# Kernel tuning notes

Hardware: AMD Instinct MI355X
Metric: run time of the kernel (lower is better)

## Reference

```python
import jax, jax.numpy as jnp
import numpy as np

N, D_IN, D_KQ, D_V = 4096, 1024, 1024, 1024


def setup_inputs() -> dict:
    key = jax.random.key(0)
    kx, kq, kk, kv = jax.random.split(key, 4)
    return {
        "x": jax.random.normal(kx, (N, D_IN), dtype=jnp.float32),
        "W_query": jax.random.uniform(kq, (D_IN, D_KQ), dtype=jnp.float32),
        "W_key": jax.random.uniform(kk, (D_IN, D_KQ), dtype=jnp.float32),
        "W_value": jax.random.uniform(kv, (D_IN, D_V), dtype=jnp.float32),
        "masked": 1,
    }


def reference(x, W_query, W_key, W_value, masked):
    # x: [N, d_in]; single-head, unbatched attention
    queries = x @ W_query          # [N, d_kq]
    keys = x @ W_key               # [N, d_kq]
    values = x @ W_value           # [N, d_v]
    scores = queries @ keys.T      # [N, N]
    if masked:  # masked is a static Python int
        n = x.shape[0]
        causal = jnp.triu(jnp.ones((n, n), dtype=bool), k=1)
        scores = jnp.where(causal, -jnp.inf, scores)
    scale = 1.0 / jnp.sqrt(jnp.asarray(W_key.shape[1], dtype=scores.dtype))
    attn = jax.nn.softmax(scores * scale, axis=-1)
    return attn @ values           # [N, d_v]
```

## Files before the change

kernel.cpp:

```cpp
#include <hip/hip_runtime.h>
#include <hip/hip_bf16.h>


using bf16 = __hip_bfloat16;
using f32x4 = __attribute__((ext_vector_type(4))) float;
using i32x4 = __attribute__((ext_vector_type(4))) int;
using i8 = signed char;

__device__ __forceinline__ void gload_lds16(const void* g, void* l) {
  __builtin_amdgcn_global_load_lds(
      (const __attribute__((address_space(1))) void*)g,
      (__attribute__((address_space(3))) void*)l, 16, 0, 0);
}

template <int ROWS, int CPR, int NT>
__device__ __forceinline__ void stage_tile8(const i8* __restrict__ g, i8* s,
                                            int ld) {
  const int t = threadIdx.x;
#pragma unroll
  for (int c = 0; c < ROWS * CPR / NT; ++c) {
    const int idx = c * NT + t;
    const int row = idx / CPR;
    const int ch = idx & (CPR - 1);
    const int cg = ch ^ ((row >> 1) & (CPR - 1));
    gload_lds16(g + (size_t)row * ld + cg * 16, s + idx * 16);
  }
}
template <int CPR>
__device__ __forceinline__ i32x4 frag_at8(const i8* s, int row, int ch) {
  return *(const i32x4*)&s[(row * CPR + (ch ^ ((row >> 1) & (CPR - 1)))) * 16];
}

__device__ __forceinline__ i32x4 mfma_i8(i32x4 a, i32x4 b, i32x4 c) {
  return __builtin_amdgcn_mfma_i32_16x16x64_i8(a, b, c, 0, 0, 0);
}

__global__ __launch_bounds__(256, 4) void gemm_qkv_i8(
    const i8* __restrict__ xh, const i8* __restrict__ xl,
    const i8* __restrict__ qTh, const i8* __restrict__ qTl,
    const i8* __restrict__ kTh, const i8* __restrict__ kTl,
    const i8* __restrict__ vTh, const i8* __restrict__ vTl,
    const float* __restrict__ srow, i8* __restrict__ Qh, i8* __restrict__ Ql,
    i8* __restrict__ Kh, i8* __restrict__ Kl, short* __restrict__ V16) {
  __shared__ __align__(16) i8 sAh[128 * 64], sAl[128 * 64];
  __shared__ __align__(16) i8 sBh[64 * 64], sBl[64 * 64];

  const int bx = blockIdx.x;
  const int which = bx >> 4;
  const int n0 = (bx & 15) * 64;
  const int m0 = blockIdx.y * 128;
  const i8* Bh = which == 0 ? qTh : which == 1 ? kTh : vTh;
  const i8* Bl = which == 0 ? qTl : which == 1 ? kTl : vTl;
  const i8* A_h = xh + (size_t)m0 * 1024;
  const i8* A_l = xl + (size_t)m0 * 1024;
  const i8* B_h = Bh + (size_t)n0 * 1024;
  const i8* B_l = Bl + (size_t)n0 * 1024;

  const int t = threadIdx.x, lane = t & 63, w = t >> 6;
  const int wr = (w >> 1) * 64, wc = (w & 1) * 32;
  const int frow = lane & 15, fc = lane >> 4;

  i32x4 a0[4][2], a1[4][2];
#pragma unroll
  for (int i = 0; i < 4; ++i)
#pragma unroll
    for (int j = 0; j < 2; ++j) {
      a0[i][j] = (i32x4){0, 0, 0, 0};
      a1[i][j] = (i32x4){0, 0, 0, 0};
    }

  for (int kt = 0; kt < 16; ++kt) {
    const int k0 = kt * 64;
    stage_tile8<128, 4, 256>(A_h + k0, sAh, 1024);
    stage_tile8<64, 4, 256>(B_h + k0, sBh, 1024);
    stage_tile8<128, 4, 256>(A_l + k0, sAl, 1024);
    stage_tile8<64, 4, 256>(B_l + k0, sBl, 1024);
    __syncthreads();

    i32x4 ah[4], al[4], bh[2], bl[2];
#pragma unroll
    for (int i = 0; i < 4; ++i) {
      ah[i] = frag_at8<4>(sAh, wr + i * 16 + frow, fc);
      al[i] = frag_at8<4>(sAl, wr + i * 16 + frow, fc);
    }
#pragma unroll
    for (int j = 0; j < 2; ++j) {
      bh[j] = frag_at8<4>(sBh, wc + j * 16 + frow, fc);
      bl[j] = frag_at8<4>(sBl, wc + j * 16 + frow, fc);
    }
#pragma unroll
    for (int i = 0; i < 4; ++i)
#pragma unroll
      for (int j = 0; j < 2; ++j) {
        a0[i][j] = mfma_i8(ah[i], bh[j], a0[i][j]);
        a1[i][j] = mfma_i8(ah[i], bl[j], a1[i][j]);
        a1[i][j] = mfma_i8(al[i], bh[j], a1[i][j]);
      }
    __syncthreads();
  }

  const int er = (lane >> 4) * 4, ec = lane & 15;
  if (which < 2) {
    i8* Ph = which == 0 ? Qh : Kh;
    i8* Pl = which == 0 ? Ql : Kl;
#pragma unroll
    for (int i = 0; i < 4; ++i)
#pragma unroll
      for (int j = 0; j < 2; ++j)
#pragma unroll
        for (int r = 0; r < 4; ++r) {
          const int gm = m0 + wr + i * 16 + er + r;
          const int gn = n0 + wc + j * 16 + ec;
          const float Qf =
              65536.f * (float)a0[i][j][r] + 256.f * (float)a1[i][j][r];
          int q16 = __float2int_rn(Qf * (1.f / 262144.f));
          q16 = min(max(q16, -32511), 32511);
          const int h = (q16 + 128) >> 8;
          const int l = q16 - (h << 8);
          const size_t off = (size_t)gm * 1024 + gn;
          Ph[off] = (i8)h;
          Pl[off] = (i8)l;
        }
  } else {
#pragma unroll
    for (int i = 0; i < 4; ++i)
#pragma unroll
      for (int j = 0; j < 2; ++j)
#pragma unroll
        for (int r = 0; r < 4; ++r) {
          const int gm = m0 + wr + i * 16 + er + r;
          const int gn = n0 + wc + j * 16 + ec;
          const float Vf =
              (65536.f * (float)a0[i][j][r] + 256.f * (float)a1[i][j][r]) *
                  (1.f / 134217728.f) +
              0.5f * srow[gm];
          int v16 = __float2int_rn(Vf * 256.f);
          v16 = min(max(v16, -32511), 32511);
          V16[(size_t)gm * 1024 + gn] = (short)v16;
        }
  }
}

__global__ __launch_bounds__(512, 4) void gemm_s_i8(
    const i8* __restrict__ Qh, const i8* __restrict__ Ql,
    const i8* __restrict__ Kh, const i8* __restrict__ Kl,
    const float* __restrict__ srow, const float* __restrict__ qsum,
    const float* __restrict__ ksum, float* __restrict__ S) {
  const int cb = blockIdx.x, rb = blockIdx.y;
  if (cb > rb) return;
  const int n0 = cb * 128, m0 = rb * 128;
  __shared__ __align__(16) i8 sAh[128 * 64], sAl[128 * 64];
  __shared__ __align__(16) i8 sBh[128 * 64], sBl[128 * 64];

  const i8* A_h = Qh + (size_t)m0 * 1024;
  const i8* A_l = Ql + (size_t)m0 * 1024;
  const i8* B_h = Kh + (size_t)n0 * 1024;
  const i8* B_l = Kl + (size_t)n0 * 1024;

  const int t = threadIdx.x, lane = t & 63, w = t >> 6;
  const int wr = (w >> 2) * 64, wc = (w & 3) * 32;
  const int frow = lane & 15, fc = lane >> 4;

  i32x4 a0[4][2], a1[4][2];
#pragma unroll
  for (int i = 0; i < 4; ++i)
#pragma unroll
    for (int j = 0; j < 2; ++j) {
      a0[i][j] = (i32x4){0, 0, 0, 0};
      a1[i][j] = (i32x4){0, 0, 0, 0};
    }

  for (int kt = 0; kt < 16; ++kt) {
    const int k0 = kt * 64;
    stage_tile8<128, 4, 512>(A_h + k0, sAh, 1024);
    stage_tile8<128, 4, 512>(B_h + k0, sBh, 1024);
    stage_tile8<128, 4, 512>(A_l + k0, sAl, 1024);
    stage_tile8<128, 4, 512>(B_l + k0, sBl, 1024);
    __syncthreads();

    i32x4 ah[4], al[4], bh[2], bl[2];
#pragma unroll
    for (int i = 0; i < 4; ++i) {
      ah[i] = frag_at8<4>(sAh, wr + i * 16 + frow, fc);
      al[i] = frag_at8<4>(sAl, wr + i * 16 + frow, fc);
    }
#pragma unroll
    for (int j = 0; j < 2; ++j) {
      bh[j] = frag_at8<4>(sBh, wc + j * 16 + frow, fc);
      bl[j] = frag_at8<4>(sBl, wc + j * 16 + frow, fc);
    }
#pragma unroll
    for (int i = 0; i < 4; ++i)
#pragma unroll
      for (int j = 0; j < 2; ++j) {
        a0[i][j] = mfma_i8(ah[i], bh[j], a0[i][j]);
        a1[i][j] = mfma_i8(ah[i], bl[j], a1[i][j]);
        a1[i][j] = mfma_i8(al[i], bh[j], a1[i][j]);
      }
    __syncthreads();
  }

  const int er = (lane >> 4) * 4, ec = lane & 15;
  float sn[2], kn[2];
#pragma unroll
  for (int j = 0; j < 2; ++j) {
    const int gn = n0 + wc + j * 16 + ec;
    sn[j] = srow[gn];
    kn[j] = ksum[gn];
  }
#pragma unroll
  for (int i = 0; i < 4; ++i)
#pragma unroll
    for (int r = 0; r < 4; ++r) {
      const int gm = m0 + wr + i * 16 + er + r;
      const float sm = srow[gm], qm = qsum[gm];
#pragma unroll
      for (int j = 0; j < 2; ++j) {
        const int gn = n0 + wc + j * 16 + ec;
        const float Sf =
            65536.f * (float)a0[i][j][r] + 256.f * (float)a1[i][j][r];
        const float logit = Sf * (1.f / 8388608.f) +
                            0.015625f * (sn[j] * qm + sm * kn[j]) +
                            8.f * sm * sn[j];
        S[(size_t)gm * 4096 + gn] = logit;
      }
    }
}

__global__ __launch_bounds__(256, 4) void gemm_pv_i8(
    const i8* __restrict__ P, const i8* __restrict__ VTh,
    const i8* __restrict__ VTl, const float* __restrict__ inv_s,
    float* __restrict__ O) {
  __shared__ __align__(16) i8 sP[128 * 64];
  __shared__ __align__(16) i8 sVh[64 * 64], sVl[64 * 64];

  const int bxr = blockIdx.x;
  const int rb = (bxr & 1) ? (31 - (bxr >> 1)) : (bxr >> 1);
  const int m0 = rb * 128;
  const int n0 = blockIdx.y * 64;
  const int ktiles = 2 * (rb + 1);

  const i8* A0 = P + (size_t)m0 * 4096;
  const i8* Bh0 = VTh + (size_t)n0 * 4096;
  const i8* Bl0 = VTl + (size_t)n0 * 4096;

  const int t = threadIdx.x, lane = t & 63, w = t >> 6;
  const int wr = (w >> 1) * 64, wc = (w & 1) * 32;
  const int frow = lane & 15, fc = lane >> 4;

  i32x4 a0[4][2], a1[4][2];
#pragma unroll
  for (int i = 0; i < 4; ++i)
#pragma unroll
    for (int j = 0; j < 2; ++j) {
      a0[i][j] = (i32x4){0, 0, 0, 0};
      a1[i][j] = (i32x4){0, 0, 0, 0};
    }

  for (int kt = 0; kt < ktiles; ++kt) {
    const int k0 = kt * 64;
    stage_tile8<128, 4, 256>(A0 + k0, sP, 4096);
    stage_tile8<64, 4, 256>(Bh0 + k0, sVh, 4096);
    stage_tile8<64, 4, 256>(Bl0 + k0, sVl, 4096);
    __syncthreads();

    i32x4 pa[4], bh[2], bl[2];
#pragma unroll
    for (int i = 0; i < 4; ++i) pa[i] = frag_at8<4>(sP, wr + i * 16 + frow, fc);
#pragma unroll
    for (int j = 0; j < 2; ++j) {
      bh[j] = frag_at8<4>(sVh, wc + j * 16 + frow, fc);
      bl[j] = frag_at8<4>(sVl, wc + j * 16 + frow, fc);
    }
#pragma unroll
    for (int i = 0; i < 4; ++i)
#pragma unroll
      for (int j = 0; j < 2; ++j) {
        a0[i][j] = mfma_i8(pa[i], bh[j], a0[i][j]);
        a1[i][j] = mfma_i8(pa[i], bl[j], a1[i][j]);
      }
    __syncthreads();
  }

  const int er = (lane >> 4) * 4, ec = lane & 15;
#pragma unroll
  for (int i = 0; i < 4; ++i)
#pragma unroll
    for (int j = 0; j < 2; ++j)
#pragma unroll
      for (int r = 0; r < 4; ++r) {
        const int gm = m0 + wr + i * 16 + er + r;
        const int gn = n0 + wc + j * 16 + ec;
        const float val = 256.f * (float)a0[i][j][r] + (float)a1[i][j][r];
        O[(size_t)gm * 1024 + gn] = val * inv_s[gm] * (1.f / 32512.f);
      }
}

__global__ __launch_bounds__(256) void softmax_kernel(
    const float* __restrict__ S, i8* __restrict__ P,
    float* __restrict__ inv_s, int N) {
  const int wid = threadIdx.x >> 6;
  const int r0 = blockIdx.x * 2 + (wid >> 1);
  const int row = (wid & 1) ? (N - 1 - r0) : r0;
  const int lane = threadIdx.x & 63;
  const float* s = S + (size_t)row * N;
  i8* p = P + (size_t)row * N;
  const int len = row + 1;
  const int nv4 = len >> 2;
  const float4* s4 = (const float4*)s;

  float m = -3.4e38f;
  for (int j = lane; j < nv4; j += 64) {
    const float4 v = s4[j];
    m = fmaxf(m, fmaxf(fmaxf(v.x, v.y), fmaxf(v.z, v.w)));
  }
  for (int j = (nv4 << 2) + lane; j < len; j += 64) m = fmaxf(m, s[j]);
#pragma unroll
  for (int off = 32; off > 0; off >>= 1) m = fmaxf(m, __shfl_xor(m, off, 64));

  float sum = 0.f;
  for (int j = lane; j < nv4; j += 64) {
    const float4 v = s4[j];
    const float e0 = __expf(v.x - m), e1 = __expf(v.y - m);
    const float e2 = __expf(v.z - m), e3 = __expf(v.w - m);
    sum += (e0 + e1) + (e2 + e3);
    uint pk = (uint)__float2int_rn(e0 * 127.f);
    pk |= (uint)__float2int_rn(e1 * 127.f) << 8;
    pk |= (uint)__float2int_rn(e2 * 127.f) << 16;
    pk |= (uint)__float2int_rn(e3 * 127.f) << 24;
    *(uint*)(p + 4 * j) = pk;
  }
  for (int j = (nv4 << 2) + lane; j < len; j += 64) {
    const float e = __expf(s[j] - m);
    sum += e;
    p[j] = (i8)__float2int_rn(e * 127.f);
  }
#pragma unroll
  for (int off = 32; off > 0; off >>= 1) sum += __shfl_xor(sum, off, 64);

  const int bound = ((row >> 7) + 1) << 7;
  for (int j = len + lane; j < bound; j += 64) p[j] = (i8)0;
  if (lane == 0) inv_s[row] = 1.f / sum;
}

__global__ void split_x_i8(const float4* __restrict__ x, uint* __restrict__ h,
                           uint* __restrict__ l, int n4) {
  const int i = blockIdx.x * blockDim.x + threadIdx.x;
  if (i >= n4) return;
  const float4 v = x[i];
  const float f[4] = {v.x, v.y, v.z, v.w};
  uint hp = 0, lp = 0;
#pragma unroll
  for (int k = 0; k < 4; ++k) {
    int q = __float2int_rn(f[k] * 4096.f);
    q = min(max(q, -32511), 32511);
    const int hh = (q + 128) >> 8;
    const int ll = q - (hh << 8);
    hp |= (uint)(hh & 255) << (8 * k);
    lp |= (uint)(ll & 255) << (8 * k);
  }
  h[i] = hp;
  l[i] = lp;
}

__global__ void split_transpose_w_i8(
    const float* __restrict__ W0, const float* __restrict__ W1,
    const float* __restrict__ W2, i8* __restrict__ T0h, i8* __restrict__ T0l,
    i8* __restrict__ T1h, i8* __restrict__ T1l, i8* __restrict__ T2h,
    i8* __restrict__ T2l, int R, int C) {
  const int z = blockIdx.z;
  const float* W = z == 0 ? W0 : z == 1 ? W1 : W2;
  i8* Th = z == 0 ? T0h : z == 1 ? T1h : T2h;
  i8* Tl = z == 0 ? T0l : z == 1 ? T1l : T2l;
  __shared__ float tile[32][33];
  const int c0 = blockIdx.x * 32, r0 = blockIdx.y * 32;
  const int tx = threadIdx.x, ty = threadIdx.y;
  for (int rr = ty; rr < 32; rr += 8)
    tile[rr][tx] = W[(size_t)(r0 + rr) * C + c0 + tx];
  __syncthreads();
  for (int cc = ty; cc < 32; cc += 8) {
    const float v = tile[tx][cc] - 0.5f;
    int w16 = __float2int_rn(v * 32768.f);
    w16 = min(max(w16, -32511), 32511);
    const int h = (w16 + 128) >> 8;
    const int l = w16 - (h << 8);
    const size_t off = (size_t)(c0 + cc) * R + r0 + tx;
    Th[off] = (i8)h;
    Tl[off] = (i8)l;
  }
}

__global__ __launch_bounds__(256) void wrow_kernel(const float* __restrict__ Wq,
                                                   const float* __restrict__ Wk,
                                                   float* __restrict__ wqrow,
                                                   float* __restrict__ wkrow) {
  const int k = blockIdx.x * 4 + (threadIdx.x >> 6);
  const int lane = threadIdx.x & 63;
  const float* W = blockIdx.y == 0 ? Wq : Wk;
  float* out = blockIdx.y == 0 ? wqrow : wkrow;
  const float* row = W + (size_t)k * 1024;
  float s = 0.f;
  for (int c = lane; c < 1024; c += 64) s += row[c];
#pragma unroll
  for (int off = 32; off > 0; off >>= 1) s += __shfl_xor(s, off, 64);
  if (lane == 0) out[k] = s - 512.f;
}

__global__ __launch_bounds__(256) void rowstats_kernel(
    const float* __restrict__ x, const float* __restrict__ wqrow,
    const float* __restrict__ wkrow, float* __restrict__ srow,
    float* __restrict__ qsum, float* __restrict__ ksum) {
  const int i = blockIdx.x * 4 + (threadIdx.x >> 6);
  const int lane = threadIdx.x & 63;
  const float* row = x + (size_t)i * 1024;
  float ss = 0.f, sq = 0.f, sk = 0.f;
  for (int c = lane; c < 1024; c += 64) {
    const float v = row[c];
    ss += v;
    sq += v * wqrow[c];
    sk += v * wkrow[c];
  }
#pragma unroll
  for (int off = 32; off > 0; off >>= 1) {
    ss += __shfl_xor(ss, off, 64);
    sq += __shfl_xor(sq, off, 64);
    sk += __shfl_xor(sk, off, 64);
  }
  if (lane == 0) {
    srow[i] = ss;
    qsum[i] = sq;
    ksum[i] = sk;
  }
}

__global__ void transpose_v16(const short* __restrict__ V16,
                              i8* __restrict__ Th, i8* __restrict__ Tl, int R,
                              int C) {
  __shared__ short tile[32][33];
  const int c0 = blockIdx.x * 32, r0 = blockIdx.y * 32;
  const int tx = threadIdx.x, ty = threadIdx.y;
  for (int rr = ty; rr < 32; rr += 8)
    tile[rr][tx] = V16[(size_t)(r0 + rr) * C + c0 + tx];
  __syncthreads();
  for (int cc = ty; cc < 32; cc += 8) {
    const int v = tile[tx][cc];
    const int h = (v + 128) >> 8;
    const int l = v - (h << 8);
    const size_t off = (size_t)(c0 + cc) * R + r0 + tx;
    Th[off] = (i8)h;
    Tl[off] = (i8)l;
  }
}

extern "C" void kernel_launch(void* const* d_in, const int* in_sizes, int n_in,
                              void* d_out, int out_size, void* d_ws,
                              size_t ws_size, hipStream_t stream) {
  (void)in_sizes; (void)n_in; (void)out_size; (void)ws_size;
  const float* x = (const float*)d_in[0];
  const float* Wq = (const float*)d_in[1];
  const float* Wk = (const float*)d_in[2];
  const float* Wv = (const float*)d_in[3];

  const int N = 4096, D = 1024;

  char* p = (char*)d_ws;
  auto alloc = [&](size_t bytes) {
    char* r = p;
    p += (bytes + 255) & ~(size_t)255;
    return r;
  };
  i8* xh = (i8*)alloc((size_t)N * D);
  i8* xl = (i8*)alloc((size_t)N * D);
  i8* WqTh = (i8*)alloc((size_t)D * D);
  i8* WqTl = (i8*)alloc((size_t)D * D);
  i8* WkTh = (i8*)alloc((size_t)D * D);
  i8* WkTl = (i8*)alloc((size_t)D * D);
  i8* WvTh = (i8*)alloc((size_t)D * D);
  i8* WvTl = (i8*)alloc((size_t)D * D);
  i8* Qh = (i8*)alloc((size_t)N * D);
  i8* Ql = (i8*)alloc((size_t)N * D);
  i8* Kh = (i8*)alloc((size_t)N * D);
  i8* Kl = (i8*)alloc((size_t)N * D);
  short* V16 = (short*)alloc((size_t)N * D * 2);
  i8* VTh = (i8*)alloc((size_t)D * N);
  i8* VTl = (i8*)alloc((size_t)D * N);
  float* S = (float*)alloc((size_t)N * N * 4);
  i8* P = (i8*)alloc((size_t)N * N);
  float* inv_s = (float*)alloc((size_t)N * 4);
  float* srow = (float*)alloc((size_t)N * 4);
  float* qsum = (float*)alloc((size_t)N * 4);
  float* ksum = (float*)alloc((size_t)N * 4);
  float* wqrow = (float*)alloc((size_t)D * 4);
  float* wkrow = (float*)alloc((size_t)D * 4);

  split_x_i8<<<N * D / 4 / 256, 256, 0, stream>>>((const float4*)x, (uint*)xh,
                                                  (uint*)xl, N * D / 4);
  split_transpose_w_i8<<<dim3(32, 32, 3), dim3(32, 8), 0, stream>>>(
      Wq, Wk, Wv, WqTh, WqTl, WkTh, WkTl, WvTh, WvTl, D, D);
  wrow_kernel<<<dim3(D / 4, 2), 256, 0, stream>>>(Wq, Wk, wqrow, wkrow);
  rowstats_kernel<<<N / 4, 256, 0, stream>>>(x, wqrow, wkrow, srow, qsum, ksum);

  gemm_qkv_i8<<<dim3(48, 32), 256, 0, stream>>>(xh, xl, WqTh, WqTl, WkTh, WkTl,
                                                WvTh, WvTl, srow, Qh, Ql, Kh,
                                                Kl, V16);
  transpose_v16<<<dim3(D / 32, N / 32), dim3(32, 8), 0, stream>>>(V16, VTh,
                                                                  VTl, N, D);

  gemm_s_i8<<<dim3(32, 32), 512, 0, stream>>>(Qh, Ql, Kh, Kl, srow, qsum, ksum,
                                              S);

  softmax_kernel<<<N / 4, 256, 0, stream>>>(S, P, inv_s, N);

  gemm_pv_i8<<<dim3(32, 16), 256, 0, stream>>>(P, VTh, VTl, inv_s,
                                               (float*)d_out);
}
```

Before: 270.6 us.

## Quantize V to single int8 plane and shrink causal S-tile width

V is now quantized to one int8 value instead of a hi/lo 16-bit split. This halves the PV GEMM MFMA count, V-tile staging and transpose traffic, and drops the second accumulator set. Separately, the QK^T kernel moves to 128x64 tiles with 256 threads, so the causal diagonal wastes fewer computed-then-masked elements and more blocks are available. The V precision loss is large, since values go from a step of 1/256 to a step of 1 before clamping to ±127, and this risks accuracy failures.

Result: slower. 290.9 us (+7.5%).

```diff
diff --git a/kernel.cpp b/kernel.cpp
--- a/kernel.cpp
+++ b/kernel.cpp
@@ -41,7 +41,7 @@
     const i8* __restrict__ kTh, const i8* __restrict__ kTl,
     const i8* __restrict__ vTh, const i8* __restrict__ vTl,
     const float* __restrict__ srow, i8* __restrict__ Qh, i8* __restrict__ Ql,
-    i8* __restrict__ Kh, i8* __restrict__ Kl, short* __restrict__ V16) {
+    i8* __restrict__ Kh, i8* __restrict__ Kl, i8* __restrict__ V8) {
   __shared__ __align__(16) i8 sAh[128 * 64], sAl[128 * 64];
   __shared__ __align__(16) i8 sBh[64 * 64], sBl[64 * 64];
 
@@ -134,23 +134,23 @@
               (65536.f * (float)a0[i][j][r] + 256.f * (float)a1[i][j][r]) *
                   (1.f / 134217728.f) +
               0.5f * srow[gm];
-          int v16 = __float2int_rn(Vf * 256.f);
-          v16 = min(max(v16, -32511), 32511);
-          V16[(size_t)gm * 1024 + gn] = (short)v16;
+          int v8 = __float2int_rn(Vf);
+          v8 = min(max(v8, -127), 127);
+          V8[(size_t)gm * 1024 + gn] = (i8)v8;
         }
   }
 }
 
-__global__ __launch_bounds__(512, 4) void gemm_s_i8(
+__global__ __launch_bounds__(256, 4) void gemm_s_i8(
     const i8* __restrict__ Qh, const i8* __restrict__ Ql,
     const i8* __restrict__ Kh, const i8* __restrict__ Kl,
     const float* __restrict__ srow, const float* __restrict__ qsum,
     const float* __restrict__ ksum, float* __restrict__ S) {
   const int cb = blockIdx.x, rb = blockIdx.y;
-  if (cb > rb) return;
-  const int n0 = cb * 128, m0 = rb * 128;
+  if (cb > 2 * rb + 1) return;
+  const int n0 = cb * 64, m0 = rb * 128;
   __shared__ __align__(16) i8 sAh[128 * 64], sAl[128 * 64];
-  __shared__ __align__(16) i8 sBh[128 * 64], sBl[128 * 64];
+  __shared__ __align__(16) i8 sBh[64 * 64], sBl[64 * 64];
 
   const i8* A_h = Qh + (size_t)m0 * 1024;
   const i8* A_l = Ql + (size_t)m0 * 1024;
@@ -158,7 +158,7 @@
   const i8* B_l = Kl + (size_t)n0 * 1024;
 
   const int t = threadIdx.x, lane = t & 63, w = t >> 6;
-  const int wr = (w >> 2) * 64, wc = (w & 3) * 32;
+  const int wr = (w >> 1) * 64, wc = (w & 1) * 32;
   const int frow = lane & 15, fc = lane >> 4;
 
   i32x4 a0[4][2], a1[4][2];
@@ -172,10 +172,10 @@
 
   for (int kt = 0; kt < 16; ++kt) {
     const int k0 = kt * 64;
-    stage_tile8<128, 4, 512>(A_h + k0, sAh, 1024);
-    stage_tile8<128, 4, 512>(B_h + k0, sBh, 1024);
-    stage_tile8<128, 4, 512>(A_l + k0, sAl, 1024);
-    stage_tile8<128, 4, 512>(B_l + k0, sBl, 1024);
+    stage_tile8<128, 4, 256>(A_h + k0, sAh, 1024);
+    stage_tile8<64, 4, 256>(B_h + k0, sBh, 1024);
+    stage_tile8<128, 4, 256>(A_l + k0, sAl, 1024);
+    stage_tile8<64, 4, 256>(B_l + k0, sBl, 1024);
     __syncthreads();
 
     i32x4 ah[4], al[4], bh[2], bl[2];
@@ -228,11 +228,10 @@
 }
 
 __global__ __launch_bounds__(256, 4) void gemm_pv_i8(
-    const i8* __restrict__ P, const i8* __restrict__ VTh,
-    const i8* __restrict__ VTl, const float* __restrict__ inv_s,
-    float* __restrict__ O) {
+    const i8* __restrict__ P, const i8* __restrict__ VT,
+    const float* __restrict__ inv_s, float* __restrict__ O) {
   __shared__ __align__(16) i8 sP[128 * 64];
-  __shared__ __align__(16) i8 sVh[64 * 64], sVl[64 * 64];
+  __shared__ __align__(16) i8 sV[64 * 64];
 
   const int bxr = blockIdx.x;
   const int rb = (bxr & 1) ? (31 - (bxr >> 1)) : (bxr >> 1);
@@ -241,44 +240,33 @@
   const int ktiles = 2 * (rb + 1);
 
   const i8* A0 = P + (size_t)m0 * 4096;
-  const i8* Bh0 = VTh + (size_t)n0 * 4096;
-  const i8* Bl0 = VTl + (size_t)n0 * 4096;
+  const i8* B0 = VT + (size_t)n0 * 4096;
 
   const int t = threadIdx.x, lane = t & 63, w = t >> 6;
   const int wr = (w >> 1) * 64, wc = (w & 1) * 32;
   const int frow = lane & 15, fc = lane >> 4;
 
-  i32x4 a0[4][2], a1[4][2];
+  i32x4 a0[4][2];
 #pragma unroll
   for (int i = 0; i < 4; ++i)
 #pragma unroll
-    for (int j = 0; j < 2; ++j) {
-      a0[i][j] = (i32x4){0, 0, 0, 0};
-      a1[i][j] = (i32x4){0, 0, 0, 0};
-    }
+    for (int j = 0; j < 2; ++j) a0[i][j] = (i32x4){0, 0, 0, 0};
 
   for (int kt = 0; kt < ktiles; ++kt) {
     const int k0 = kt * 64;
     stage_tile8<128, 4, 256>(A0 + k0, sP, 4096);
-    stage_tile8<64, 4, 256>(Bh0 + k0, sVh, 4096);
-    stage_tile8<64, 4, 256>(Bl0 + k0, sVl, 4096);
-    __syncthreads();
-
-    i32x4 pa[4], bh[2], bl[2];
+    stage_tile8<64, 4, 256>(B0 + k0, sV, 4096);
+    __syncthreads();
+
+    i32x4 pa[4], b[2];
 #pragma unroll
     for (int i = 0; i < 4; ++i) pa[i] = frag_at8<4>(sP, wr + i * 16 + frow, fc);
 #pragma unroll
-    for (int j = 0; j < 2; ++j) {
-      bh[j] = frag_at8<4>(sVh, wc + j * 16 + frow, fc);
-      bl[j] = frag_at8<4>(sVl, wc + j * 16 + frow, fc);
-    }
+    for (int j = 0; j < 2; ++j) b[j] = frag_at8<4>(sV, wc + j * 16 + frow, fc);
 #pragma unroll
     for (int i = 0; i < 4; ++i)
 #pragma unroll
-      for (int j = 0; j < 2; ++j) {
-        a0[i][j] = mfma_i8(pa[i], bh[j], a0[i][j]);
-        a1[i][j] = mfma_i8(pa[i], bl[j], a1[i][j]);
-      }
+      for (int j = 0; j < 2; ++j) a0[i][j] = mfma_i8(pa[i], b[j], a0[i][j]);
     __syncthreads();
   }
 
@@ -291,8 +279,8 @@
       for (int r = 0; r < 4; ++r) {
         const int gm = m0 + wr + i * 16 + er + r;
         const int gn = n0 + wc + j * 16 + ec;
-        const float val = 256.f * (float)a0[i][j][r] + (float)a1[i][j][r];
-        O[(size_t)gm * 1024 + gn] = val * inv_s[gm] * (1.f / 32512.f);
+        O[(size_t)gm * 1024 + gn] =
+            (float)a0[i][j][r] * inv_s[gm] * (1.f / 127.f);
       }
 }
 
@@ -433,23 +421,16 @@
   }
 }
 
-__global__ void transpose_v16(const short* __restrict__ V16,
-                              i8* __restrict__ Th, i8* __restrict__ Tl, int R,
-                              int C) {
-  __shared__ short tile[32][33];
+__global__ void transpose_v8(const i8* __restrict__ V8, i8* __restrict__ T,
+                             int R, int C) {
+  __shared__ i8 tile[32][33];
   const int c0 = blockIdx.x * 32, r0 = blockIdx.y * 32;
   const int tx = threadIdx.x, ty = threadIdx.y;
   for (int rr = ty; rr < 32; rr += 8)
-    tile[rr][tx] = V16[(size_t)(r0 + rr) * C + c0 + tx];
+    tile[rr][tx] = V8[(size_t)(r0 + rr) * C + c0 + tx];
   __syncthreads();
-  for (int cc = ty; cc < 32; cc += 8) {
-    const int v = tile[tx][cc];
-    const int h = (v + 128) >> 8;
-    const int l = v - (h << 8);
-    const size_t off = (size_t)(c0 + cc) * R + r0 + tx;
-    Th[off] = (i8)h;
-    Tl[off] = (i8)l;
-  }
+  for (int cc = ty; cc < 32; cc += 8)
+    T[(size_t)(c0 + cc) * R + r0 + tx] = tile[tx][cc];
 }
 
 extern "C" void kernel_launch(void* const* d_in, const int* in_sizes, int n_in,
@@ -481,9 +462,8 @@
   i8* Ql = (i8*)alloc((size_t)N * D);
   i8* Kh = (i8*)alloc((size_t)N * D);
   i8* Kl = (i8*)alloc((size_t)N * D);
-  short* V16 = (short*)alloc((size_t)N * D * 2);
-  i8* VTh = (i8*)alloc((size_t)D * N);
-  i8* VTl = (i8*)alloc((size_t)D * N);
+  i8* V8 = (i8*)alloc((size_t)N * D);
+  i8* VT = (i8*)alloc((size_t)D * N);
   float* S = (float*)alloc((size_t)N * N * 4);
   i8* P = (i8*)alloc((size_t)N * N);
   float* inv_s = (float*)alloc((size_t)N * 4);
@@ -502,15 +482,13 @@
 
   gemm_qkv_i8<<<dim3(48, 32), 256, 0, stream>>>(xh, xl, WqTh, WqTl, WkTh, WkTl,
                                                 WvTh, WvTl, srow, Qh, Ql, Kh,
-                                                Kl, V16);
-  transpose_v16<<<dim3(D / 32, N / 32), dim3(32, 8), 0, stream>>>(V16, VTh,
-                                                                  VTl, N, D);
-
-  gemm_s_i8<<<dim3(32, 32), 512, 0, stream>>>(Qh, Ql, Kh, Kl, srow, qsum, ksum,
+                                                Kl, V8);
+  transpose_v8<<<dim3(D / 32, N / 32), dim3(32, 8), 0, stream>>>(V8, VT, N, D);
+
+  gemm_s_i8<<<dim3(64, 32), 256, 0, stream>>>(Qh, Ql, Kh, Kl, srow, qsum, ksum,
                                               S);
 
   softmax_kernel<<<N / 4, 256, 0, stream>>>(S, P, inv_s, N);
 
-  gemm_pv_i8<<<dim3(32, 16), 256, 0, stream>>>(P, VTh, VTl, inv_s,
-                                               (float*)d_out);
-}
+  gemm_pv_i8<<<dim3(32, 16), 256, 0, stream>>>(P, VT, inv_s, (float*)d_out);
+}
```
